# Optimization experiments

Measured on AMD Instinct MI355X. Metric: run time of the kernel, lower is better.

## Reference

```python
import jax, jax.numpy as jnp
import numpy as np

D_MODEL, D_STATE, D_CONV, EXPAND = 1024, 16, 4, 2
D_INNER = EXPAND * D_MODEL           # 2048
DT_RANK = D_MODEL // 16              # 64
BATCH, SEQLEN = 2, 2048


def setup_inputs() -> dict:
    key = jax.random.key(0)
    ks = jax.random.split(key, 10)
    s = 0.02
    hidden_states = jax.random.normal(ks[0], (BATCH, SEQLEN, D_MODEL), jnp.float32)
    in_proj_w = jax.random.normal(ks[1], (2 * D_INNER, D_MODEL), jnp.float32) * s
    conv_w = jax.random.normal(ks[2], (D_INNER, 1, D_CONV), jnp.float32) * 0.3
    conv_b = jax.random.normal(ks[3], (D_INNER,), jnp.float32) * 0.1
    x_proj_w = jax.random.normal(ks[4], (DT_RANK + 2 * D_STATE, D_INNER), jnp.float32) * s
    dt_init_std = DT_RANK ** -0.5
    dt_proj_w = jax.random.uniform(ks[5], (D_INNER, DT_RANK), jnp.float32,
                                   minval=-dt_init_std, maxval=dt_init_std)
    # bias = inverse-softplus of dt sampled log-uniform in [1e-3, 1e-1]
    dt = jnp.exp(jax.random.uniform(ks[6], (D_INNER,), jnp.float32)
                 * (np.log(0.1) - np.log(0.001)) + np.log(0.001))
    dt = jnp.clip(dt, 1e-4, None)
    dt_proj_b = dt + jnp.log(-jnp.expm1(-dt))
    # A = repeat(arange(1, d_state+1), 'n -> d n')
    A_log = jnp.log(jnp.tile(jnp.arange(1, D_STATE + 1, dtype=jnp.float32), (D_INNER, 1)))
    Dp = jnp.ones((D_INNER,), jnp.float32)
    out_proj_w = jax.random.normal(ks[7], (D_MODEL, D_INNER), jnp.float32) * s
    return {
        'hidden_states': hidden_states, 'in_proj_w': in_proj_w,
        'conv_w': conv_w, 'conv_b': conv_b, 'x_proj_w': x_proj_w,
        'dt_proj_w': dt_proj_w, 'dt_proj_b': dt_proj_b,
        'A_log': A_log, 'D': Dp, 'out_proj_w': out_proj_w,
    }


def _mamba_fwd(hidden_states, in_proj_w, conv_w, conv_b, x_proj_w,
               dt_proj_w, dt_proj_b, A_log, D, out_proj_w):
    d_inner = in_proj_w.shape[0] // 2
    d_conv = conv_w.shape[-1]
    dt_rank = dt_proj_w.shape[1]
    d_state = A_log.shape[1]
    b = hidden_states.shape[0]

    # in_proj then split into x / z gate branches  -> [B, L, d_inner] each
    xz = hidden_states @ in_proj_w.T
    x, z = jnp.split(xz, 2, axis=-1)

    # depthwise causal conv1d + SiLU (pad left d_conv-1 == padding=d_conv-1 then trim)
    xc = x.transpose(0, 2, 1)                       # [B, d_inner, L]
    xc = jax.lax.conv_general_dilated(
        xc, conv_w, window_strides=(1,), padding=[(d_conv - 1, 0)],
        dimension_numbers=('NCH', 'OIH', 'NCH'), feature_group_count=d_inner)
    xl = jax.nn.silu(xc + conv_b[None, :, None]).transpose(0, 2, 1)  # [B, L, d_inner]

    # x_proj -> dt, B, C
    x_dbl = xl @ x_proj_w.T                         # [B, L, dt_rank + 2*d_state]
    dt, Bm, Cm = jnp.split(x_dbl, [dt_rank, dt_rank + d_state], axis=-1)
    delta = jax.nn.softplus(dt @ dt_proj_w.T + dt_proj_b)  # [B, L, d_inner]

    A = -jnp.exp(A_log)                             # [d_inner, d_state]

    def step(h, inputs):
        u_t, d_t, b_t, c_t = inputs  # [B,d_inner], [B,d_inner], [B,d_state], [B,d_state]
        dA = jnp.exp(d_t[..., None] * A)                      # [B, d_inner, d_state]
        h = dA * h + (d_t * u_t)[..., None] * b_t[:, None, :]
        y_t = jnp.einsum('bdn,bn->bd', h, c_t)
        return h, y_t

    h0 = jnp.zeros((b, d_inner, d_state), hidden_states.dtype)
    xs = (xl.transpose(1, 0, 2), delta.transpose(1, 0, 2),
          Bm.transpose(1, 0, 2), Cm.transpose(1, 0, 2))
    _, ys = jax.lax.scan(step, h0, xs)              # ys: [L, B, d_inner]
    y = ys.transpose(1, 0, 2)

    y = y + xl * D                                  # skip (D) term
    y = y * jax.nn.silu(z)                          # gate
    return y @ out_proj_w.T                         # [B, L, d_model]


def reference(hidden_states, in_proj_w, conv_w, conv_b, x_proj_w,
              dt_proj_w, dt_proj_b, A_log, D, out_proj_w):
    return _mamba_fwd(hidden_states, in_proj_w, conv_w, conv_b, x_proj_w,
                      dt_proj_w, dt_proj_b, A_log, D, out_proj_w)
```

## Files before the change

### kernel.cpp

```cpp
#include <hip/hip_runtime.h>

#define D_MODEL 1024
#define D_STATE 16
#define D_CONV  4
#define D_INNER 2048
#define DT_RANK 64
#define BATCH   2
#define SEQLEN  2048
#define NTOK    (BATCH * SEQLEN)
#define NCH     64
#define LC      (SEQLEN / NCH)
#define XKS     8
#define XNC     96


__device__ __forceinline__ float bf2f(unsigned short v) {
    union { unsigned int u; float f; } c; c.u = ((unsigned int)v) << 16; return c.f;
}
__device__ __forceinline__ unsigned short f2bf(float f) {
    union { unsigned int u; float f; } c; c.f = f;
    unsigned int r = c.u + 0x7FFF + ((c.u >> 16) & 1);
    return (unsigned short)(r >> 16);
}

__device__ __forceinline__ int sniff_bf(const void* Dp) {
    return (((const unsigned int*)Dp)[0] == 0x3F803F80u) ? 1 : 0;
}

__device__ __forceinline__ float ldF(const void* p, size_t idx, int isbf) {
    return isbf ? bf2f(((const unsigned short*)p)[idx]) : ((const float*)p)[idx];
}
__device__ __forceinline__ void ld16f(const float* p, float* o) {
#pragma unroll
    for (int q = 0; q < 4; q++) {
        float4 v = *(const float4*)(p + 4 * q);
        o[4 * q + 0] = v.x; o[4 * q + 1] = v.y; o[4 * q + 2] = v.z; o[4 * q + 3] = v.w;
    }
}

#define CVT_N0 (NTOK * D_MODEL)
#define CVT_N1 (2 * D_INNER * D_MODEL)
#define CVT_N2 (D_MODEL * D_INNER)
#define CVT_N3 (D_INNER * DT_RANK)
#define CVT_TOT (CVT_N0 + CVT_N1 + CVT_N2 + CVT_N3)

__device__ __forceinline__ void cvt8(const void* in, unsigned short* out,
                                     size_t e0, int isbf)
{
    if (isbf) {
        *(uint4*)(out + e0) = *(const uint4*)((const unsigned short*)in + e0);
    } else {
        const float* f = (const float*)in + e0;
        float4 a = *(const float4*)f;
        float4 b = *(const float4*)(f + 4);
        ushort4 o0 = { f2bf(a.x), f2bf(a.y), f2bf(a.z), f2bf(a.w) };
        ushort4 o1 = { f2bf(b.x), f2bf(b.y), f2bf(b.z), f2bf(b.w) };
        *(ushort4*)(out + e0)     = o0;
        *(ushort4*)(out + e0 + 4) = o1;
    }
}

__launch_bounds__(256)
__global__ void cvt_all(const void* __restrict__ hid, const void* __restrict__ ipw,
                        const void* __restrict__ opw, const void* __restrict__ dtw,
                        unsigned short* __restrict__ hidB, unsigned short* __restrict__ ipwB,
                        unsigned short* __restrict__ opwB, unsigned short* __restrict__ dtwB,
                        const void* __restrict__ Dp)
{
    const int isbf = sniff_bf(Dp);
    size_t e = ((size_t)blockIdx.x * 256 + threadIdx.x) * 8;
    if (e < CVT_N0) { cvt8(hid, hidB, e, isbf); return; }
    e -= CVT_N0;
    if (e < CVT_N1) { cvt8(ipw, ipwB, e, isbf); return; }
    e -= CVT_N1;
    if (e < CVT_N2) { cvt8(opw, opwB, e, isbf); return; }
    e -= CVT_N2;
    if (e < CVT_N3) { cvt8(dtw, dtwB, e, isbf); }
}

typedef __attribute__((ext_vector_type(8))) __bf16 bf16x8;
typedef __attribute__((ext_vector_type(4))) float  f32x4;

__global__ void mfma_probe(int* __restrict__ dmap) {
    __shared__ alignas(16) unsigned short As[16 * 32];
    __shared__ alignas(16) unsigned short Bs[16 * 32];
    const int t = threadIdx.x;
    const int q = t >> 4, l15 = t & 15;

    for (int idx = t; idx < 512; idx += 64) {
        As[idx] = f2bf((float)(idx >> 5));
        Bs[idx] = f2bf(0.03125f);
    }
    __syncthreads();
    bf16x8 a1 = *(const bf16x8*)&As[l15 * 32 + q * 8];
    bf16x8 b1 = *(const bf16x8*)&Bs[l15 * 32 + q * 8];
    f32x4 acc1 = {0.f, 0.f, 0.f, 0.f};
    acc1 = __builtin_amdgcn_mfma_f32_16x16x32_bf16(a1, b1, acc1, 0, 0, 0);
    __syncthreads();

    for (int idx = t; idx < 512; idx += 64) {
        As[idx] = f2bf(0.03125f);
        Bs[idx] = f2bf((float)(idx >> 5));
    }
    __syncthreads();
    bf16x8 a2 = *(const bf16x8*)&As[l15 * 32 + q * 8];
    bf16x8 b2 = *(const bf16x8*)&Bs[l15 * 32 + q * 8];
    f32x4 acc2 = {0.f, 0.f, 0.f, 0.f};
    acc2 = __builtin_amdgcn_mfma_f32_16x16x32_bf16(a2, b2, acc2, 0, 0, 0);

#pragma unroll
    for (int r = 0; r < 4; r++) {
        int ma = (int)(acc1[r] + 0.5f);
        int nb = (int)(acc2[r] + 0.5f);
        if (ma < 0 || ma > 15 || nb < 0 || nb > 15) { ma = q * 4 + r; nb = l15; }
        dmap[t * 4 + r] = ma | (nb << 4);
    }
}

__device__ __forceinline__ void gl2lds16(const void* g, void* l) {
    __builtin_amdgcn_global_load_lds(
        (const __attribute__((address_space(1))) unsigned int*)g,
        (__attribute__((address_space(3))) unsigned int*)l,
        16, 0, 0);
}

__device__ __forceinline__ void stage_half(const unsigned short* __restrict__ G,
                                           int grow0, int K, int k0,
                                           unsigned short* ldsAB, int half, int t)
{
    const int r8  = t >> 3;
    const int c8  = t & 7;
    const int swz = (c8 ^ (r8 & 7)) << 3;
#pragma unroll
    for (int j = 0; j < 2; j++) {
        const int row = half * 128 + j * 64 + r8;
        gl2lds16(&G[(size_t)(grow0 + row) * K + k0 + swz],
                 &ldsAB[row * 64 + c8 * 8]);
    }
}

__device__ __forceinline__ bf16x8 ldsfrag(const unsigned short* p, int row, int slot) {
    return *(const bf16x8*)&p[row * 64 + ((slot ^ (row & 7)) << 3)];
}

__launch_bounds__(512)
__global__ void gemm1_8ph(const unsigned short* __restrict__ A,
                          const unsigned short* __restrict__ B,
                          float* __restrict__ C,
                          int M, int N, int K,
                          const int* __restrict__ dmap)
{
    extern __shared__ __align__(16) unsigned short lds[];
    unsigned short* A0l = lds;
    unsigned short* B0l = lds + 16384;
    unsigned short* A1l = lds + 32768;
    unsigned short* B1l = lds + 49152;

    const int t    = threadIdx.x;
    const int lane = t & 63;
    const int w    = t >> 6;
    const int wm   = (w >> 2) * 128, wn = (w & 3) * 64;
    const int q    = lane >> 4, l15 = lane & 15;

    const int nbn  = N >> 8;
    const int nwg  = (M >> 8) * nbn;
    const int orig = blockIdx.x;
    const int wg   = (orig & 7) * (nwg >> 3) + (orig >> 3);
    const int bm   = wg / nbn, bn = wg % nbn;
    const int m0   = bm << 8, n0 = bn << 8;
    const int NT   = K >> 6;

    int mp[4];
#pragma unroll
    for (int r = 0; r < 4; r++) mp[r] = dmap[lane * 4 + r];

    f32x4 acc[8][4];
#pragma unroll
    for (int i = 0; i < 8; i++)
#pragma unroll
        for (int j = 0; j < 4; j++) acc[i][j] = (f32x4){0.f, 0.f, 0.f, 0.f};

    stage_half(B, n0, K, 0, B0l, 0, t);
    stage_half(B, n0, K, 0, B0l, 1, t);
    stage_half(A, m0, K, 0, A0l, 0, t);
    stage_half(A, m0, K, 0, A0l, 1, t);
    {
        const int k1 = (NT > 1 ? 64 : 0);
        stage_half(B, n0, K, k1, B1l, 0, t);
        stage_half(B, n0, K, k1, B1l, 1, t);
    }
    asm volatile("s_waitcnt vmcnt(4)" ::: "memory");
    __builtin_amdgcn_s_barrier();

#pragma unroll 2
    for (int tt = 0; tt < NT; ++tt) {
        const int p = tt & 1;
        const unsigned short* Ac = p ? A1l : A0l;
        const unsigned short* Bc = p ? B1l : B0l;
        unsigned short* Anx = p ? A0l : A1l;
        unsigned short* Bnx = p ? B1l : B0l;
        const int kA = (tt + 1 < NT ? tt + 1 : 0) << 6;
        const int kB = (tt + 2 < NT ? tt + 2 : 0) << 6;

        bf16x8 af[4][2], b0r[2][2], b1r[2][2];

#pragma unroll
        for (int i = 0; i < 4; i++)
#pragma unroll
            for (int ks = 0; ks < 2; ks++)
                af[i][ks] = ldsfrag(Ac, wm + i * 16 + l15, ks * 4 + q);
#pragma unroll
        for (int j = 0; j < 2; j++)
#pragma unroll
            for (int ks = 0; ks < 2; ks++)
                b0r[j][ks] = ldsfrag(Bc, wn + j * 16 + l15, ks * 4 + q);
        stage_half(A, m0, K, kA, Anx, 0, t);
        asm volatile("" ::: "memory");
        __builtin_amdgcn_s_barrier();
        __builtin_amdgcn_s_setprio(1);
#pragma unroll
        for (int i = 0; i < 4; i++)
#pragma unroll
            for (int j = 0; j < 2; j++)
#pragma unroll
                for (int ks = 0; ks < 2; ks++)
                    acc[i][j] = __builtin_amdgcn_mfma_f32_16x16x32_bf16(
                        af[i][ks], b0r[j][ks], acc[i][j], 0, 0, 0);
        __builtin_amdgcn_s_setprio(0);
        asm volatile("" ::: "memory");
        __builtin_amdgcn_s_barrier();

#pragma unroll
        for (int j = 0; j < 2; j++)
#pragma unroll
            for (int ks = 0; ks < 2; ks++)
                b1r[j][ks] = ldsfrag(Bc, wn + 32 + j * 16 + l15, ks * 4 + q);
        stage_half(A, m0, K, kA, Anx, 1, t);
        asm volatile("" ::: "memory");
        __builtin_amdgcn_s_barrier();
        __builtin_amdgcn_s_setprio(1);
#pragma unroll
        for (int i = 0; i < 4; i++)
#pragma unroll
            for (int j = 0; j < 2; j++)
#pragma unroll
                for (int ks = 0; ks < 2; ks++)
                    acc[i][2 + j] = __builtin_amdgcn_mfma_f32_16x16x32_bf16(
                        af[i][ks], b1r[j][ks], acc[i][2 + j], 0, 0, 0);
        __builtin_amdgcn_s_setprio(0);
        asm volatile("" ::: "memory");
        __builtin_amdgcn_s_barrier();

#pragma unroll
        for (int i = 0; i < 4; i++)
#pragma unroll
            for (int ks = 0; ks < 2; ks++)
                af[i][ks] = ldsfrag(Ac, wm + 64 + i * 16 + l15, ks * 4 + q);
        stage_half(B, n0, K, kB, Bnx, 0, t);
        asm volatile("" ::: "memory");
        __builtin_amdgcn_s_barrier();
        __builtin_amdgcn_s_setprio(1);
#pragma unroll
        for (int i = 0; i < 4; i++)
#pragma unroll
            for (int j = 0; j < 2; j++)
#pragma unroll
                for (int ks = 0; ks < 2; ks++)
                    acc[4 + i][2 + j] = __builtin_amdgcn_mfma_f32_16x16x32_bf16(
                        af[i][ks], b1r[j][ks], acc[4 + i][2 + j], 0, 0, 0);
        __builtin_amdgcn_s_setprio(0);
        asm volatile("" ::: "memory");
        __builtin_amdgcn_s_barrier();

        stage_half(B, n0, K, kB, Bnx, 1, t);
        asm volatile("" ::: "memory");
        __builtin_amdgcn_s_barrier();
        __builtin_amdgcn_s_setprio(1);
#pragma unroll
        for (int i = 0; i < 4; i++)
#pragma unroll
            for (int j = 0; j < 2; j++)
#pragma unroll
                for (int ks = 0; ks < 2; ks++)
                    acc[4 + i][j] = __builtin_amdgcn_mfma_f32_16x16x32_bf16(
                        af[i][ks], b0r[j][ks], acc[4 + i][j], 0, 0, 0);
        __builtin_amdgcn_s_setprio(0);
        asm volatile("s_waitcnt vmcnt(4)" ::: "memory");
        __builtin_amdgcn_s_barrier();
    }

#pragma unroll
    for (int i = 0; i < 8; i++) {
#pragma unroll
        for (int r = 0; r < 4; r++) {
            const int mo = mp[r] & 15, no = mp[r] >> 4;
            const int m = m0 + wm + i * 16 + mo;
#pragma unroll
            for (int j = 0; j < 4; j++) {
                const int n = n0 + wn + j * 16 + no;
                C[(size_t)m * N + n] = acc[i][j][r];
            }
        }
    }
}

template<int EPI, int NJ, int SWAP>
__launch_bounds__(256)
__global__ void gemm_mfma_bt(const unsigned short* __restrict__ A,
                             const unsigned short* __restrict__ B,
                             float* __restrict__ C,
                             int M, int N, int K,
                             const int* __restrict__ dmap,
                             const void* __restrict__ bias,
                             const void* __restrict__ Dp)
{
    constexpr int BN = NJ * 32;
    __shared__ alignas(16) unsigned short As[128 * 32];
    __shared__ alignas(16) unsigned short Bs[BN * 32];
    const int t    = threadIdx.x;
    const int lane = t & 63;
    const int w    = t >> 6;
    const int bm   = SWAP ? blockIdx.x : blockIdx.y;
    const int bn   = SWAP ? blockIdx.y : blockIdx.x;
    const int m0   = bm * 128, n0 = bn * BN;
    const int wm   = (w >> 1) * 64, wn = (w & 1) * (NJ * 16);
    const int q    = lane >> 4, l15 = lane & 15;

    int mp[4];
#pragma unroll
    for (int r = 0; r < 4; r++) mp[r] = dmap[lane * 4 + r];

    const int srow = t >> 2;
    const int skk  = (t & 3) * 8;

    f32x4 acc[4][NJ];
#pragma unroll
    for (int i = 0; i < 4; i++)
#pragma unroll
        for (int j = 0; j < NJ; j++) acc[i][j] = (f32x4){0.f, 0.f, 0.f, 0.f};

    for (int k0 = 0; k0 < K; k0 += 32) {
        __syncthreads();
        gl2lds16(&A[(size_t)(m0 +      srow) * K + k0 + skk], &As[(     srow) * 32 + skk]);
        gl2lds16(&A[(size_t)(m0 + 64 + srow) * K + k0 + skk], &As[(64 + srow) * 32 + skk]);
#pragma unroll
        for (int jb = 0; jb < NJ / 2; jb++)
            gl2lds16(&B[(size_t)(n0 + jb * 64 + srow) * K + k0 + skk],
                     &Bs[(jb * 64 + srow) * 32 + skk]);
        __syncthreads();

        bf16x8 af[4], bfr[NJ];
#pragma unroll
        for (int i = 0; i < 4; i++)
            af[i] = *(const bf16x8*)&As[(wm + i * 16 + l15) * 32 + q * 8];
#pragma unroll
        for (int j = 0; j < NJ; j++)
            bfr[j] = *(const bf16x8*)&Bs[(wn + j * 16 + l15) * 32 + q * 8];
#pragma unroll
        for (int i = 0; i < 4; i++)
#pragma unroll
            for (int j = 0; j < NJ; j++)
                acc[i][j] = __builtin_amdgcn_mfma_f32_16x16x32_bf16(
                    af[i], bfr[j], acc[i][j], 0, 0, 0);
    }

    const int isbf = EPI ? sniff_bf(Dp) : 0;
#pragma unroll
    for (int i = 0; i < 4; i++) {
#pragma unroll
        for (int r = 0; r < 4; r++) {
            const int mo = mp[r] & 15, no = mp[r] >> 4;
            const int m = m0 + wm + i * 16 + mo;
#pragma unroll
            for (int j = 0; j < NJ; j++) {
                const int n = n0 + wn + j * 16 + no;
                float v = acc[i][j][r];
                if (EPI == 1) {
                    v += ldF(bias, n, isbf);
                    v = fmaxf(v, 0.f) + __logf(1.f + __expf(-fabsf(v)));
                }
                C[(size_t)m * N + n] = v;
            }
        }
    }
}

__launch_bounds__(256)
__global__ void xproj_splitk(const float* __restrict__ A,
                             const float* __restrict__ B,
                             float* __restrict__ part)
{
    __shared__ alignas(16) float As[16][68];
    __shared__ alignas(16) float Bs[16][68];
    const int t  = threadIdx.x;
    const int m0 = blockIdx.y * 64, n0 = blockIdx.x * 64;
    const int koff = blockIdx.z * (D_INNER / XKS);
    const int lr = t >> 2;
    const int lk = (t & 3) * 4;
    const int tm = t >> 4, tn = t & 15;

    float acc[4][4];
#pragma unroll
    for (int i = 0; i < 4; i++)
#pragma unroll
        for (int j = 0; j < 4; j++) acc[i][j] = 0.f;

    for (int k0 = koff; k0 < koff + D_INNER / XKS; k0 += 16) {
        float av[4], bv[4];
        {
            const int m = m0 + lr;
            float4 p = *(const float4*)&A[(size_t)m * D_INNER + k0 + lk];
            av[0] = p.x; av[1] = p.y; av[2] = p.z; av[3] = p.w;
        }
        {
            const int n = n0 + lr;
            if (n < XNC) {
                float4 p = *(const float4*)&B[(size_t)n * D_INNER + k0 + lk];
                bv[0] = p.x; bv[1] = p.y; bv[2] = p.z; bv[3] = p.w;
            } else { bv[0] = bv[1] = bv[2] = bv[3] = 0.f; }
        }
        __syncthreads();
#pragma unroll
        for (int i = 0; i < 4; i++) { As[lk + i][lr] = av[i]; Bs[lk + i][lr] = bv[i]; }
        __syncthreads();

#pragma unroll
        for (int kk = 0; kk < 16; kk++) {
            float4 a = *(const float4*)&As[kk][tm * 4];
            float4 b = *(const float4*)&Bs[kk][tn * 4];
            float aa[4] = { a.x, a.y, a.z, a.w };
            float bb[4] = { b.x, b.y, b.z, b.w };
#pragma unroll
            for (int i = 0; i < 4; i++)
#pragma unroll
                for (int j = 0; j < 4; j++) acc[i][j] = fmaf(aa[i], bb[j], acc[i][j]);
        }
    }

    float* out = part + (size_t)blockIdx.z * NTOK * XNC;
#pragma unroll
    for (int i = 0; i < 4; i++) {
        const int m = m0 + tm * 4 + i;
#pragma unroll
        for (int j = 0; j < 4; j++) {
            const int n = n0 + tn * 4 + j;
            if (n < XNC) out[(size_t)m * XNC + n] = acc[i][j];
        }
    }
}

__launch_bounds__(256)
__global__ void xproj_reduce(const float* __restrict__ part, float* __restrict__ xdbl,
                             unsigned short* __restrict__ xdt)
{
    const int idx = blockIdx.x * 256 + threadIdx.x;
    float s = 0.f;
#pragma unroll
    for (int z = 0; z < XKS; z++) s += part[(size_t)z * NTOK * XNC + idx];
    xdbl[idx] = s;
    const int m = idx / XNC;
    const int col = idx - m * XNC;
    if (col < 64) xdt[m * 64 + col] = f2bf(s);
}

__launch_bounds__(256)
__global__ void conv_silu(const float* __restrict__ xz,
                          const void* __restrict__ conv_w,
                          const void* __restrict__ conv_b,
                          float* __restrict__ xl,
                          const void* __restrict__ Dp)
{
    const int isbf = sniff_bf(Dp);
    const int gid = blockIdx.x * 256 + threadIdx.x;
    const int dq  = gid & (D_INNER / 4 - 1);
    const int tg  = gid >> 9;
    const int d0  = dq * 4;
    const int tok0 = tg * 4;
    const int l0  = tok0 & (SEQLEN - 1);

    float w[4][4], bias[4];
#pragma unroll
    for (int dd = 0; dd < 4; dd++) {
        bias[dd] = ldF(conv_b, d0 + dd, isbf);
#pragma unroll
        for (int j = 0; j < 4; j++) w[dd][j] = ldF(conv_w, (d0 + dd) * 4 + j, isbf);
    }

    float4 x[7];
    const float* rowp = xz + (size_t)tok0 * (2 * D_INNER) + d0;
#pragma unroll
    for (int k = 0; k < 7; k++) {
        const int off = k - 3;
        if (l0 + off >= 0)
            x[k] = *(const float4*)(rowp + (ptrdiff_t)off * (2 * D_INNER));
        else
            x[k] = (float4){0.f, 0.f, 0.f, 0.f};
    }

#pragma unroll
    for (int tn = 0; tn < 4; tn++) {
        float a0 = bias[0], a1 = bias[1], a2 = bias[2], a3 = bias[3];
#pragma unroll
        for (int j = 0; j < 4; j++) {
            const float4 v = x[tn + j];
            a0 = fmaf(v.x, w[0][j], a0);
            a1 = fmaf(v.y, w[1][j], a1);
            a2 = fmaf(v.z, w[2][j], a2);
            a3 = fmaf(v.w, w[3][j], a3);
        }
        float4 o;
        o.x = a0 / (1.f + __expf(-a0));
        o.y = a1 / (1.f + __expf(-a1));
        o.z = a2 / (1.f + __expf(-a2));
        o.w = a3 / (1.f + __expf(-a3));
        *(float4*)&xl[(size_t)(tok0 + tn) * D_INNER + d0] = o;
    }
}

__device__ __forceinline__ void mk_dA(float dv, const float An[16], int pw, float* dA)
{
    if (pw) {
        const float E = __expf(dv * An[0]);
        dA[0] = E;
        const float E2 = E * E;          dA[1] = E2;
        const float E4 = E2 * E2;        dA[3] = E4;
        const float E8 = E4 * E4;        dA[7] = E8;
        dA[2]  = E2 * E;
        dA[4]  = E4 * E;   dA[5]  = E4 * E2;  dA[6]  = dA[5] * E;
        dA[8]  = E8 * E;   dA[9]  = E8 * E2;  dA[10] = dA[9] * E;
        dA[11] = E8 * E4;  dA[12] = dA[11] * E;
        dA[13] = dA[11] * E2; dA[14] = dA[13] * E; dA[15] = E8 * E8;
    } else {
#pragma unroll
        for (int n = 0; n < 16; n++) dA[n] = __expf(dv * An[n]);
    }
}

__device__ __forceinline__ int chk_pw(const float An[16])
{
    int pw = 1;
#pragma unroll
    for (int n = 1; n < 16; n++)
        pw = pw && (fabsf(An[n] - (float)(n + 1) * An[0]) <= 3e-4f * (float)(n + 1));
    return pw;
}

__device__ __forceinline__ void scan_step(float h[16], float dv, float uv,
                                          const float Bv[16], const float An[16], int pw)
{
    float dA[16]; mk_dA(dv, An, pw, dA);
    const float du = dv * uv;
#pragma unroll
    for (int n = 0; n < 16; n++) h[n] = fmaf(dA[n], h[n], du * Bv[n]);
}

__device__ __forceinline__ float scan_step_y(float h[16], float dv, float uv,
                                             const float Bv[16], const float Cv[16],
                                             const float An[16], int pw, float Dd)
{
    float dA[16]; mk_dA(dv, An, pw, dA);
    const float du = dv * uv;
    float s[16];
#pragma unroll
    for (int n = 0; n < 16; n++) {
        h[n] = fmaf(dA[n], h[n], du * Bv[n]);
        s[n] = h[n] * Cv[n];
    }
#pragma unroll
    for (int n = 0; n < 8; n++) s[n] += s[n + 8];
#pragma unroll
    for (int n = 0; n < 4; n++) s[n] += s[n + 4];
    s[0] += s[2]; s[1] += s[3];
    return s[0] + s[1] + uv * Dd;
}

__launch_bounds__(256)
__global__ void scan_chunk(const float* __restrict__ dlt,
                           const float* __restrict__ xl,
                           const float* __restrict__ xdbl,
                           const void* __restrict__ A_log,
                           float* __restrict__ S,
                           float* __restrict__ sumD,
                           const void* __restrict__ Dp)
{
    const int isbf = sniff_bf(Dp);
    const int t  = threadIdx.x;
    const int dg = blockIdx.x & 7;
    const int c  = (blockIdx.x >> 3) & (NCH - 1);
    const int b  = blockIdx.x >> 9;
    const int d  = dg * 256 + t;

    float An[16], h[16];
#pragma unroll
    for (int n = 0; n < 16; n++) {
        An[n] = -expf(ldF(A_log, d * 16 + n, isbf));
        h[n] = 0.f;
    }
    const int pw = chk_pw(An);
    float sd = 0.f;
    const size_t r0 = (size_t)b * SEQLEN + c * LC;

    float dv0 = dlt[r0 * D_INNER + d];
    float uv0 = xl [r0 * D_INNER + d];
    float Bv0[16]; ld16f(&xdbl[r0 * 96 + 64], Bv0);

    for (int i = 0; i < LC; i += 2) {
        const size_t r1 = r0 + i + 1;
        float dv1 = dlt[r1 * D_INNER + d];
        float uv1 = xl [r1 * D_INNER + d];
        float Bv1[16]; ld16f(&xdbl[r1 * 96 + 64], Bv1);

        scan_step(h, dv0, uv0, Bv0, An, pw);
        sd += dv0;

        const size_t r2 = r0 + ((i + 2 < LC) ? (i + 2) : (i + 1));
        dv0 = dlt[r2 * D_INNER + d];
        uv0 = xl [r2 * D_INNER + d];
        ld16f(&xdbl[r2 * 96 + 64], Bv0);

        scan_step(h, dv1, uv1, Bv1, An, pw);
        sd += dv1;
    }

    const size_t base = (((size_t)b * NCH + c) * 16) * D_INNER + d;
#pragma unroll
    for (int n = 0; n < 16; n++) S[base + (size_t)n * D_INNER] = h[n];
    sumD[((size_t)b * NCH + c) * D_INNER + d] = sd;
}

__launch_bounds__(256)
__global__ void scan_combine(float* __restrict__ S,
                             const float* __restrict__ sumD,
                             const void* __restrict__ A_log,
                             const void* __restrict__ Dp)
{
    const int isbf = sniff_bf(Dp);
    const int g = blockIdx.x * 256 + threadIdx.x;
    const int d = g & (D_INNER - 1);
    const int n = (g >> 11) & 15;
    const int b = g >> 15;
    const float An = -expf(ldF(A_log, d * 16 + n, isbf));

    float hs = 0.f;
    float Sc = S[(((size_t)b * NCH + 0) * 16 + n) * D_INNER + d];
    float sd = sumD[((size_t)b * NCH + 0) * D_INNER + d];
    for (int c = 0; c < NCH; c++) {
        const int cn = (c + 1 < NCH) ? c + 1 : c;
        const float Scn = S[(((size_t)b * NCH + cn) * 16 + n) * D_INNER + d];
        const float sdn = sumD[((size_t)b * NCH + cn) * D_INNER + d];
        S[(((size_t)b * NCH + c) * 16 + n) * D_INNER + d] = hs;
        hs = fmaf(__expf(An * sd), hs, Sc);
        Sc = Scn; sd = sdn;
    }
}

__launch_bounds__(256)
__global__ void scan_apply(const float* __restrict__ dlt,
                           const float* __restrict__ xl,
                           const float* __restrict__ xdbl,
                           const float* __restrict__ xz,
                           const void* __restrict__ A_log,
                           const void* __restrict__ Dp,
                           const float* __restrict__ S,
                           unsigned short* __restrict__ yg)
{
    const int isbf = sniff_bf(Dp);
    const int t  = threadIdx.x;
    const int dg = blockIdx.x & 7;
    const int c  = (blockIdx.x >> 3) & (NCH - 1);
    const int b  = blockIdx.x >> 9;
    const int d  = dg * 256 + t;

    float An[16], h[16];
    const size_t base = (((size_t)b * NCH + c) * 16) * D_INNER + d;
#pragma unroll
    for (int n = 0; n < 16; n++) {
        An[n] = -expf(ldF(A_log, d * 16 + n, isbf));
        h[n] = S[base + (size_t)n * D_INNER];
    }
    const int pw = chk_pw(An);
    const float Dd = ldF(Dp, d, isbf);
    const size_t r0 = (size_t)b * SEQLEN + c * LC;

    float dv0 = dlt[r0 * D_INNER + d];
    float uv0 = xl [r0 * D_INNER + d];
    float zv0 = xz [r0 * (2 * D_INNER) + D_INNER + d];
    float Bv0[16], Cv0[16];
    ld16f(&xdbl[r0 * 96 + 64], Bv0);
    ld16f(&xdbl[r0 * 96 + 80], Cv0);

    for (int i = 0; i < LC; i += 2) {
        const size_t ra = r0 + i + 1;
        float dv1 = dlt[ra * D_INNER + d];
        float uv1 = xl [ra * D_INNER + d];
        float zv1 = xz [ra * (2 * D_INNER) + D_INNER + d];
        float Bv1[16], Cv1[16];
        ld16f(&xdbl[ra * 96 + 64], Bv1);
        ld16f(&xdbl[ra * 96 + 80], Cv1);

        {
            const float yv = scan_step_y(h, dv0, uv0, Bv0, Cv0, An, pw, Dd);
            yg[(r0 + i) * D_INNER + d] = f2bf(yv * (zv0 / (1.f + expf(-zv0))));
        }

        const size_t rb = r0 + ((i + 2 < LC) ? (i + 2) : (i + 1));
        dv0 = dlt[rb * D_INNER + d];
        uv0 = xl [rb * D_INNER + d];
        zv0 = xz [rb * (2 * D_INNER) + D_INNER + d];
        ld16f(&xdbl[rb * 96 + 64], Bv0);
        ld16f(&xdbl[rb * 96 + 80], Cv0);

        {
            const float yv = scan_step_y(h, dv1, uv1, Bv1, Cv1, An, pw, Dd);
            yg[ra * D_INNER + d] = f2bf(yv * (zv1 / (1.f + expf(-zv1))));
        }
    }
}

extern "C" void kernel_launch(void* const* d_in, const int* in_sizes, int n_in,
                              void* d_out, int out_size, void* d_ws, size_t ws_size,
                              hipStream_t stream)
{
    const void* hidden     = d_in[0];
    const void* in_proj_w  = d_in[1];
    const void* conv_w     = d_in[2];
    const void* conv_b     = d_in[3];
    const void* x_proj_w   = d_in[4];
    const void* dt_proj_w  = d_in[5];
    const void* dt_proj_b  = d_in[6];
    const void* A_log      = d_in[7];
    const void* Dp         = d_in[8];
    const void* out_proj_w = d_in[9];

    char* ws = (char*)d_ws;
    float*          xz   = (float*)(ws);
    float*          xl   = (float*)(ws + 67108864ull);
    float*          xdbl = (float*)(ws + 100663296ull);
    float*          dlt  = (float*)(ws + 102236160ull);
    unsigned short* yg   = (unsigned short*)(ws + 135790592ull);
    unsigned short* opwB = (unsigned short*)(ws + 152567808ull);
    unsigned short* xdt  = (unsigned short*)(ws + 156762112ull);
    unsigned short* dtwB = (unsigned short*)(ws + 157286400ull);
    float*          S    = (float*)(ws + 169345280ull);
    float*          sumD = (float*)(ws + 186122496ull);
    int*            dmap = (int*)  (ws + 187171072ull);
    unsigned short* hidB  = (unsigned short*)(ws + 102236160ull);
    unsigned short* ipwB  = (unsigned short*)(ws + 102236160ull + 8388608ull);
    float*          xpart = (float*)(ws + 102236160ull);

    dim3 blk(256);

    mfma_probe<<<dim3(1), dim3(64), 0, stream>>>(dmap);

    cvt_all<<<dim3(CVT_TOT / (256 * 8)), blk, 0, stream>>>(
        hidden, in_proj_w, out_proj_w, dt_proj_w, hidB, ipwB, opwB, dtwB, Dp);

    hipFuncSetAttribute((const void*)gemm1_8ph,
                        hipFuncAttributeMaxDynamicSharedMemorySize, 131072);
    gemm1_8ph<<<dim3((NTOK / 256) * (2 * D_INNER / 256)), dim3(512), 131072, stream>>>(
        hidB, ipwB, xz, NTOK, 2 * D_INNER, D_MODEL, dmap);

    conv_silu<<<dim3((NTOK / 4) * (D_INNER / 4) / 256), blk, 0, stream>>>(
        xz, conv_w, conv_b, xl, Dp);

    xproj_splitk<<<dim3(2, 64, XKS), blk, 0, stream>>>(
        xl, (const float*)x_proj_w, xpart);
    xproj_reduce<<<dim3(NTOK * XNC / 256), blk, 0, stream>>>(xpart, xdbl, xdt);

    gemm_mfma_bt<1, 4, 0><<<dim3(16, 32), blk, 0, stream>>>(
        xdt, dtwB, dlt, NTOK, D_INNER, DT_RANK, dmap, dt_proj_b, Dp);

    scan_chunk<<<dim3(BATCH * NCH * (D_INNER / 256)), blk, 0, stream>>>(
        dlt, xl, xdbl, A_log, S, sumD, Dp);
    scan_combine<<<dim3(BATCH * 16 * D_INNER / 256), blk, 0, stream>>>(
        S, sumD, A_log, Dp);
    scan_apply<<<dim3(BATCH * NCH * (D_INNER / 256)), blk, 0, stream>>>(
        dlt, xl, xdbl, xz, A_log, Dp, S, yg);

    gemm_mfma_bt<0, 2, 1><<<dim3(32, 16), blk, 0, stream>>>(
        yg, opwB, (float*)d_out, NTOK, D_MODEL, D_INNER, dmap, nullptr, Dp);
}
```

Before: 330.0 us.

## Add dedicated double-buffered out-proj GEMM with XCD-aware tile remapping

Replaces the generic templated GEMM used for the output projection with a specialized kernel. The new kernel uses 128x64 tiles, a two-stage LDS double buffer with direct global-to-LDS loads and an XOR-swizzled layout. It also remaps block IDs across the 8 XCDs so that neighbouring tiles share L2. The aim is to overlap loads with MFMA work and improve cache locality for this shape. The cost is fewer accumulators per wave and a full vmcnt(0) wait every iteration, which may limit the overlap.

```diff
diff --git a/kernel.cpp b/kernel.cpp
--- a/kernel.cpp
+++ b/kernel.cpp
@@ -297,6 +297,132 @@
             const int m = m0 + wm + i * 16 + mo;
 #pragma unroll
             for (int j = 0; j < 4; j++) {
+                const int n = n0 + wn + j * 16 + no;
+                C[(size_t)m * N + n] = acc[i][j][r];
+            }
+        }
+    }
+}
+
+__device__ __forceinline__ void stage_op(const unsigned short* __restrict__ A,
+                                         const unsigned short* __restrict__ B,
+                                         int m0, int n0, int K, int k0,
+                                         unsigned short* Al, unsigned short* Bl, int t)
+{
+    const int r   = t >> 3;
+    const int c8  = t & 7;
+    const int swz = (c8 ^ (r & 7)) << 3;
+#pragma unroll
+    for (int j = 0; j < 4; j++) {
+        const int row = j * 32 + r;
+        gl2lds16(&A[(size_t)(m0 + row) * K + k0 + swz], &Al[row * 64 + c8 * 8]);
+    }
+#pragma unroll
+    for (int j = 0; j < 2; j++) {
+        const int row = j * 32 + r;
+        gl2lds16(&B[(size_t)(n0 + row) * K + k0 + swz], &Bl[row * 64 + c8 * 8]);
+    }
+}
+
+__launch_bounds__(256)
+__global__ void gemm_op_2ph(const unsigned short* __restrict__ A,
+                            const unsigned short* __restrict__ B,
+                            float* __restrict__ C,
+                            const int* __restrict__ dmap)
+{
+    constexpr int M = NTOK, N = D_MODEL, K = D_INNER;
+    constexpr int NT = K / 64;
+    __shared__ alignas(16) unsigned short Al[2][128 * 64];
+    __shared__ alignas(16) unsigned short Bl[2][64 * 64];
+
+    const int t    = threadIdx.x;
+    const int lane = t & 63;
+    const int w    = t >> 6;
+    const int wm   = (w >> 1) * 64, wn = (w & 1) * 32;
+    const int q    = lane >> 4, l15 = lane & 15;
+
+    const int nbn  = N / 64;
+    const int nwg  = (M / 128) * nbn;
+    const int orig = blockIdx.x;
+    const int wg   = (orig & 7) * (nwg >> 3) + (orig >> 3);
+    const int bm   = wg / nbn, bn = wg % nbn;
+    const int m0   = bm * 128, n0 = bn * 64;
+
+    int mp[4];
+#pragma unroll
+    for (int r = 0; r < 4; r++) mp[r] = dmap[lane * 4 + r];
+
+    f32x4 acc[4][2];
+#pragma unroll
+    for (int i = 0; i < 4; i++)
+#pragma unroll
+        for (int j = 0; j < 2; j++) acc[i][j] = (f32x4){0.f, 0.f, 0.f, 0.f};
+
+    stage_op(A, B, m0, n0, K, 0, Al[0], Bl[0], t);
+    asm volatile("s_waitcnt vmcnt(0)" ::: "memory");
+    __builtin_amdgcn_s_barrier();
+
+#pragma unroll 2
+    for (int tt = 0; tt < NT - 1; ++tt) {
+        const int cur = tt & 1;
+        stage_op(A, B, m0, n0, K, (tt + 1) * 64, Al[cur ^ 1], Bl[cur ^ 1], t);
+
+        bf16x8 af[4][2], bfr[2][2];
+#pragma unroll
+        for (int i = 0; i < 4; i++)
+#pragma unroll
+            for (int ks = 0; ks < 2; ks++)
+                af[i][ks] = ldsfrag(Al[cur], wm + i * 16 + l15, ks * 4 + q);
+#pragma unroll
+        for (int j = 0; j < 2; j++)
+#pragma unroll
+            for (int ks = 0; ks < 2; ks++)
+                bfr[j][ks] = ldsfrag(Bl[cur], wn + j * 16 + l15, ks * 4 + q);
+        __builtin_amdgcn_s_setprio(1);
+#pragma unroll
+        for (int i = 0; i < 4; i++)
+#pragma unroll
+            for (int j = 0; j < 2; j++)
+#pragma unroll
+                for (int ks = 0; ks < 2; ks++)
+                    acc[i][j] = __builtin_amdgcn_mfma_f32_16x16x32_bf16(
+                        af[i][ks], bfr[j][ks], acc[i][j], 0, 0, 0);
+        __builtin_amdgcn_s_setprio(0);
+        asm volatile("s_waitcnt vmcnt(0)" ::: "memory");
+        __builtin_amdgcn_s_barrier();
+    }
+
+    {
+        const int cur = (NT - 1) & 1;
+        bf16x8 af[4][2], bfr[2][2];
+#pragma unroll
+        for (int i = 0; i < 4; i++)
+#pragma unroll
+            for (int ks = 0; ks < 2; ks++)
+                af[i][ks] = ldsfrag(Al[cur], wm + i * 16 + l15, ks * 4 + q);
+#pragma unroll
+        for (int j = 0; j < 2; j++)
+#pragma unroll
+            for (int ks = 0; ks < 2; ks++)
+                bfr[j][ks] = ldsfrag(Bl[cur], wn + j * 16 + l15, ks * 4 + q);
+#pragma unroll
+        for (int i = 0; i < 4; i++)
+#pragma unroll
+            for (int j = 0; j < 2; j++)
+#pragma unroll
+                for (int ks = 0; ks < 2; ks++)
+                    acc[i][j] = __builtin_amdgcn_mfma_f32_16x16x32_bf16(
+                        af[i][ks], bfr[j][ks], acc[i][j], 0, 0, 0);
+    }
+
+#pragma unroll
+    for (int i = 0; i < 4; i++) {
+#pragma unroll
+        for (int r = 0; r < 4; r++) {
+            const int mo = mp[r] & 15, no = mp[r] >> 4;
+            const int m = m0 + wm + i * 16 + mo;
+#pragma unroll
+            for (int j = 0; j < 2; j++) {
                 const int n = n0 + wn + j * 16 + no;
                 C[(size_t)m * N + n] = acc[i][j][r];
             }
@@ -777,6 +903,6 @@
     scan_apply<<<dim3(BATCH * NCH * (D_INNER / 256)), blk, 0, stream>>>(
         dlt, xl, xdbl, xz, A_log, Dp, S, yg);
 
-    gemm_mfma_bt<0, 2, 1><<<dim3(32, 16), blk, 0, stream>>>(
-        yg, opwB, (float*)d_out, NTOK, D_MODEL, D_INNER, dmap, nullptr, Dp);
-}
+    gemm_op_2ph<<<dim3((NTOK / 128) * (D_MODEL / 64)), blk, 0, stream>>>(
+        yg, opwB, (float*)d_out, dmap);
+}
```

Result: faster. 317.5 us (-3.8%).
